# Kernel tuning notes

Measured on AMD Instinct MI355X. Metric: run time of the kernel, lower is better.

Reference implementation:

```python
import math
import jax, jax.numpy as jnp
import numpy as np

B, T, C = 2, 2048, 2048
H, G = 16, 4
D = C // H  # head_dim = 128
KV = G * D
SOFT_CAP = 50.0
EPS = 1e-6


def setup_inputs() -> dict:
    key = jax.random.key(0)
    ks = jax.random.split(key, 5)
    s = 1.0 / math.sqrt(C)
    return {
        "x": jax.random.normal(ks[0], (B, T, C), jnp.float32),
        "Wq": jax.random.normal(ks[1], (C, C), jnp.float32) * s,
        "Wk": jax.random.normal(ks[2], (KV, C), jnp.float32) * s,
        "Wv": jax.random.normal(ks[3], (KV, C), jnp.float32) * s,
        "Wo": jax.random.normal(ks[4], (C, C), jnp.float32) * s,
        "bo": jnp.zeros((C,), jnp.float32),
        "q_norm_w": jnp.ones((D,), jnp.float32),
        "k_norm_w": jnp.ones((D,), jnp.float32),
    }


def _rmsnorm(x, w):
    # norm/sqrt(d) formulation, eps added to rms (matches torch module exactly)
    rms = jnp.linalg.norm(x, axis=-1, keepdims=True) / math.sqrt(x.shape[-1])
    return w * (x / (rms + EPS))


def _rotary_tables(seq_len, dim):
    inv_freq = 1.0 / (10000.0 ** (jnp.arange(0, dim, 2, dtype=jnp.float32) / dim))
    t = jnp.arange(seq_len, dtype=jnp.float32)
    freqs = jnp.outer(t, inv_freq)  # [T, D/2]
    return jnp.cos(freqs), jnp.sin(freqs)


def _apply_rope(x, cos, sin):
    # x: [B, T, h, D]; cos/sin: [T, D/2] broadcast as [1, T, 1, D/2]
    d = x.shape[-1] // 2
    x1, x2 = x[..., :d], x[..., d:]
    c = cos[None, :, None, :]
    s = sin[None, :, None, :]
    return jnp.concatenate([x1 * c + x2 * s, -x1 * s + x2 * c], axis=-1)


def reference(x, Wq, Wk, Wv, Wo, bo, q_norm_w, k_norm_w):
    b, t, c = x.shape
    q = (x @ Wq.T).reshape(b, t, H, D)
    k = (x @ Wk.T).reshape(b, t, G, D)
    v = (x @ Wv.T).reshape(b, t, G, D)

    cos, sin = _rotary_tables(t, D)
    q = _apply_rope(_rmsnorm(q, q_norm_w), cos, sin)
    k = _apply_rope(_rmsnorm(k, k_norm_w), cos, sin)

    q = q.transpose(0, 2, 1, 3)              # [B, H, T, D]
    k = jnp.repeat(k.transpose(0, 2, 1, 3), H // G, axis=1)  # [B, H, T, D]
    v = jnp.repeat(v.transpose(0, 2, 1, 3), H // G, axis=1)

    att = jnp.einsum("bhqd,bhkd->bhqk", q, k) / math.sqrt(D)
    causal = jnp.tril(jnp.ones((t, t), bool))
    att = jnp.where(causal[None, None], att, -jnp.inf)
    att = SOFT_CAP * jnp.tanh(att / SOFT_CAP)  # masked entries -> -50
    att = jax.nn.softmax(att, axis=-1)

    y = jnp.einsum("bhqk,bhkd->bhqd", att, v)
    y = y.transpose(0, 2, 1, 3).reshape(b, t, c)
    return y @ Wo.T + bo
```

## Files before the change

kernel.cpp:

```cpp
#include <hip/hip_runtime.h>
#include <math.h>

#define T_SEQ 2048
#define C_DIM 2048
#define NH    16
#define NG    4
#define DH    128
#define BATCH 2

typedef unsigned short u16;
typedef __bf16 bf16_t;
typedef bf16_t bf16x8 __attribute__((ext_vector_type(8)));
typedef float  f32x4  __attribute__((ext_vector_type(4)));

static __device__ __forceinline__ u16 f2bf(float f) {
    return __builtin_bit_cast(u16, (__bf16)f);
}

static __device__ __forceinline__ void gll16(const void* g, void* lds) {
    __builtin_amdgcn_global_load_lds(
        (const __attribute__((address_space(1))) void*)(unsigned long long)(g),
        (__attribute__((address_space(3))) void*)(unsigned int)(unsigned long long)(lds),
        16, 0, 0);
}

__global__ __launch_bounds__(256)
void cast_multi(const float* __restrict__ x,  const float* __restrict__ wq,
                const float* __restrict__ wk, const float* __restrict__ wv,
                u16* __restrict__ xo, u16* __restrict__ wqo,
                u16* __restrict__ wko, u16* __restrict__ wvo) {
    int i = blockIdx.x * 256 + threadIdx.x;
    const float* src; u16* dst; int off;
    if (i < 1048576)      { src = x;  dst = xo;  off = i; }
    else if (i < 1572864) { src = wq; dst = wqo; off = i - 1048576; }
    else if (i < 1703936) { src = wk; dst = wko; off = i - 1572864; }
    else                  { src = wv; dst = wvo; off = i - 1703936; }
    const float4* p = (const float4*)src + (size_t)off * 2;
    float4 a = p[0], b = p[1];
    u16 u[8] = {f2bf(a.x), f2bf(a.y), f2bf(a.z), f2bf(a.w),
                f2bf(b.x), f2bf(b.y), f2bf(b.z), f2bf(b.w)};
    *(uint4*)(dst + (size_t)off * 8) = *(const uint4*)u;
}

__global__ __launch_bounds__(256)
void cast_f32_bf16(const float* __restrict__ in, u16* __restrict__ out, int n8) {
    int i = blockIdx.x * 256 + threadIdx.x;
    if (i >= n8) return;
    const float4* p = (const float4*)in + (size_t)i * 2;
    float4 a = p[0], b = p[1];
    u16 u[8] = {f2bf(a.x), f2bf(a.y), f2bf(a.z), f2bf(a.w),
                f2bf(b.x), f2bf(b.y), f2bf(b.z), f2bf(b.w)};
    *(uint4*)(out + (size_t)i * 8) = *(const uint4*)u;
}

__global__ __launch_bounds__(256)
void rope_tables(float* __restrict__ cosT, float* __restrict__ sinT) {
    int i = blockIdx.x * 256 + threadIdx.x;
    int tp = i >> 6, ln = i & 63;
    float invfreq = __builtin_amdgcn_exp2f(-(float)ln * (13.287712379549449f / 64.0f));
    float s, c;
    sincosf((float)tp * invfreq, &s, &c);
    cosT[i] = c;
    sinT[i] = s;
}

static __device__ __forceinline__ void gemm_body(
        u16* As, u16* Bs,
        const u16* __restrict__ A, const u16* __restrict__ B,
        const float* __restrict__ bias, float* __restrict__ C,
        int N, int K, int m0, int n0) {
    const int t    = threadIdx.x;
    const int lane = t & 63, w = t >> 6;
    const int l15  = lane & 15, quad = lane >> 4;
    const int wr   = w >> 1, wc = w & 1;

    f32x4 acc[4][4];
#pragma unroll
    for (int mt = 0; mt < 4; ++mt)
#pragma unroll
        for (int nt = 0; nt < 4; ++nt) acc[mt][nt] = (f32x4){0.f, 0.f, 0.f, 0.f};

    const int off0 = w*2048 + lane*16;
    const int r0 = off0 >> 6,          c0 = (off0 & 63) >> 1;
    const int r1 = (off0+1024) >> 6,   c1 = ((off0+1024) & 63) >> 1;
    const u16* Ag0 = A + (size_t)(m0 + r0) * K + c0;
    const u16* Ag1 = A + (size_t)(m0 + r1) * K + c1;
    const u16* Bg0 = B + (size_t)(n0 + r0) * K + c0;
    const u16* Bg1 = B + (size_t)(n0 + r1) * K + c1;
    char* AsB = (char*)As; char* BsB = (char*)Bs;
    const int ldsOff0 = w*2048, ldsOff1 = w*2048 + 1024;

    for (int k0 = 0; k0 < K; k0 += 32) {
        gll16(Ag0 + k0, AsB + ldsOff0);
        gll16(Ag1 + k0, AsB + ldsOff1);
        gll16(Bg0 + k0, BsB + ldsOff0);
        gll16(Bg1 + k0, BsB + ldsOff1);
        __syncthreads();
        bf16x8 af[4], bf[4];
#pragma unroll
        for (int mt = 0; mt < 4; ++mt)
            af[mt] = __builtin_bit_cast(bf16x8,
                *(const uint4*)&As[(wr*64 + mt*16 + l15)*32 + quad*8]);
#pragma unroll
        for (int nt = 0; nt < 4; ++nt)
            bf[nt] = __builtin_bit_cast(bf16x8,
                *(const uint4*)&Bs[(wc*64 + nt*16 + l15)*32 + quad*8]);
#pragma unroll
        for (int mt = 0; mt < 4; ++mt)
#pragma unroll
            for (int nt = 0; nt < 4; ++nt)
                acc[mt][nt] = __builtin_amdgcn_mfma_f32_16x16x32_bf16(
                                  af[mt], bf[nt], acc[mt][nt], 0, 0, 0);
        __syncthreads();
    }

#pragma unroll
    for (int mt = 0; mt < 4; ++mt)
#pragma unroll
        for (int nt = 0; nt < 4; ++nt) {
            const int col = n0 + wc*64 + nt*16 + l15;
            const float bv = bias ? bias[col] : 0.f;
#pragma unroll
            for (int r = 0; r < 4; ++r) {
                const int row = m0 + wr*64 + mt*16 + quad*4 + r;
                C[(size_t)row * N + col] = acc[mt][nt][r] + bv;
            }
        }
}

__global__ __launch_bounds__(256)
void gemm_nt_bf16(const u16* __restrict__ A, const u16* __restrict__ B,
                  const float* __restrict__ bias, float* __restrict__ C,
                  int N, int K) {
    __shared__ __align__(16) u16 As[128*32];
    __shared__ __align__(16) u16 Bs[128*32];
    gemm_body(As, Bs, A, B, bias, C, N, K, blockIdx.y*128, blockIdx.x*128);
}

__global__ __launch_bounds__(256)
void gemm_qkv(const u16* __restrict__ A,  const u16* __restrict__ Bq,
              const u16* __restrict__ Bk, const u16* __restrict__ Bv,
              float* __restrict__ Cq, float* __restrict__ Ck, float* __restrict__ Cv) {
    __shared__ __align__(16) u16 As[128*32];
    __shared__ __align__(16) u16 Bs[128*32];
    const int bx = blockIdx.x;
    const u16* B; float* C; int N, n0;
    if (bx < 16)      { B = Bq; C = Cq; N = 2048; n0 = bx * 128; }
    else if (bx < 20) { B = Bk; C = Ck; N = 512;  n0 = (bx-16) * 128; }
    else              { B = Bv; C = Cv; N = 512;  n0 = (bx-20) * 128; }
    gemm_body(As, Bs, A, B, nullptr, C, N, 2048, blockIdx.y*128, n0);
}

__global__ __launch_bounds__(256)
void rmsnorm_rope_qk(const float* __restrict__ qf, const float* __restrict__ kf,
                     const float* __restrict__ qw, const float* __restrict__ kw,
                     const float* __restrict__ cosT, const float* __restrict__ sinT,
                     u16* __restrict__ qo, u16* __restrict__ ko) {
    const int blk  = blockIdx.x;
    const int sub  = threadIdx.x >> 6;
    const int lane = threadIdx.x & 63;
    const float* in; const float* w; u16* out; int row, nheads; float scale;
    if (blk < 16384) {
        in = qf; w = qw; out = qo; nheads = NH; scale = 0.08838834764831845f;
        row = blk * 4 + sub;
    } else {
        in = kf; w = kw; out = ko; nheads = NG; scale = 1.0f;
        row = (blk - 16384) * 4 + sub;
    }
    const float* p = in + (size_t)row * 128;
    float x1 = p[lane], x2 = p[lane + 64];
    float ss = x1*x1 + x2*x2;
#pragma unroll
    for (int off = 32; off >= 1; off >>= 1) ss += __shfl_xor(ss, off, 64);
    float inv = 1.0f / (sqrtf(ss * (1.0f/128.0f)) + 1e-6f);
    float x1n = w[lane]      * x1 * inv;
    float x2n = w[lane + 64] * x2 * inv;
    int tpos = (row / nheads) & (T_SEQ - 1);
    float c = cosT[tpos*64 + lane];
    float s = sinT[tpos*64 + lane];
    out[(size_t)row*128 + lane]      = f2bf((x1n * c + x2n * s) * scale);
    out[(size_t)row*128 + lane + 64] = f2bf((x2n * c - x1n * s) * scale);
}

__global__ __launch_bounds__(256)
void v_cast_transpose(const float* __restrict__ v, u16* __restrict__ vt) {
    __shared__ u16 Lt[128 * 66];
    const int t  = threadIdx.x;
    const int t0 = blockIdx.x * 64;
    const int bg = blockIdx.y;
    const int b  = bg / NG, g = bg % NG;
#pragma unroll
    for (int rep = 0; rep < 8; ++rep) {
        int idx = rep * 256 + t;
        int i   = idx >> 5;
        int c   = idx & 31;
        float4 f = *(const float4*)(v + ((size_t)(b*T_SEQ + t0 + i)*NG + g)*DH + c*4);
        Lt[(c*4+0)*66 + i] = f2bf(f.x);
        Lt[(c*4+1)*66 + i] = f2bf(f.y);
        Lt[(c*4+2)*66 + i] = f2bf(f.z);
        Lt[(c*4+3)*66 + i] = f2bf(f.w);
    }
    __syncthreads();
#pragma unroll
    for (int rep = 0; rep < 4; ++rep) {
        int idx = rep * 256 + t;
        int d = idx >> 3, c = idx & 7;
        const u16* src = &Lt[d*66 + c*8];
        uint4 val;
        val.x = *(const unsigned int*)(src + 0);
        val.y = *(const unsigned int*)(src + 2);
        val.z = *(const unsigned int*)(src + 4);
        val.w = *(const unsigned int*)(src + 6);
        *(uint4*)(vt + ((size_t)(bg*DH + d))*T_SEQ + t0 + c*8) = val;
    }
}

__global__ __launch_bounds__(256, 2)
void flash_attn_mfma(const u16* __restrict__ qh, const u16* __restrict__ kh,
                     const u16* __restrict__ vt, u16* __restrict__ y) {
    __shared__ __align__(16) u16 Ks[2][64*128];
    __shared__ __align__(16) u16 Vs[2][128*64];

    const int t    = threadIdx.x;
    const int lane = t & 63, w = t >> 6;
    const int l15  = lane & 15, quad = lane >> 4;
    const int bg   = blockIdx.y;
    const int b    = bg >> 2, g = bg & 3;
    const int chunk = b ? (int)blockIdx.x : (63 - (int)blockIdx.x);
    const int q0   = chunk * 32;
    const int h    = g * (NH / NG) + w;

    const float C0 =  1.4426950408889634f;
    const float C1 = -0.48089834696298777f;
    const float C2 =  0.19235933878519512f;
    const float C3 = -0.07785972536301652f;

    bf16x8 aq[2][4];
#pragma unroll
    for (int m = 0; m < 2; ++m) {
        const u16* qp = qh + ((size_t)(b*T_SEQ + q0 + m*16 + l15) * NH + h) * DH;
#pragma unroll
        for (int kc = 0; kc < 4; ++kc)
            aq[m][kc] = __builtin_bit_cast(bf16x8, *(const uint4*)(qp + kc*32 + quad*8));
    }

    f32x4 accO[2][8];
#pragma unroll
    for (int m = 0; m < 2; ++m)
#pragma unroll
        for (int nd = 0; nd < 8; ++nd) accO[m][nd] = (f32x4){0.f, 0.f, 0.f, 0.f};
    float ls[2] = {0.f, 0.f};

    const u16* kgb = kh + ((size_t)b*T_SEQ*NG + g)*DH;
    const u16* vgb = vt + ((size_t)(b*NG + g)*DH)*T_SEQ;

    const int krb = t >> 4, kcl = t & 15;
    const int vdb = t >> 3, vcl = t & 7;

    const int ktiles = q0/64 + 1;

#pragma unroll
    for (int j = 0; j < 4; ++j) {
        const int kr = j*16 + krb;
        const int rp = kr & 31;
        const int kphys = (kr & 32) + ((rp >> 2) & 3)*8 + (rp >> 4)*4 + (rp & 3);
        gll16(kgb + (size_t)kphys*(NG*DH) + ((kcl ^ (kr & 7)) << 3),
              (char*)Ks[0] + j*4096 + w*1024);
        const int vd = j*32 + vdb;
        gll16(vgb + (size_t)vd*T_SEQ + ((vcl ^ (vd & 7)) << 3),
              (char*)Vs[0] + j*4096 + w*1024);
    }

    for (int kt = 0; kt < ktiles; ++kt) {
        asm volatile("s_waitcnt vmcnt(0)" ::: "memory");
        __syncthreads();

        if (kt + 1 < ktiles) {
            const int k0n = (kt + 1) * 64, bn = (kt + 1) & 1;
#pragma unroll
            for (int j = 0; j < 4; ++j) {
                const int kr = j*16 + krb;
                const int rp = kr & 31;
                const int kphys = (kr & 32) + ((rp >> 2) & 3)*8 + (rp >> 4)*4 + (rp & 3);
                gll16(kgb + (size_t)(k0n + kphys)*(NG*DH) + ((kcl ^ (kr & 7)) << 3),
                      (char*)Ks[bn] + j*4096 + w*1024);
                const int vd = j*32 + vdb;
                gll16(vgb + (size_t)vd*T_SEQ + k0n + ((vcl ^ (vd & 7)) << 3),
                      (char*)Vs[bn] + j*4096 + w*1024);
            }
        }

        const u16* Kb = Ks[kt & 1];
        const u16* Vb = Vs[kt & 1];
        const int k0 = kt * 64;
        const bool diag = (kt == ktiles - 1);

        bf16x8 pa[2][2];
#pragma unroll
        for (int b32 = 0; b32 < 2; ++b32) {
            alignas(16) u16 pk0[8];
            alignas(16) u16 pk1[8];
#pragma unroll
            for (int sub = 0; sub < 2; ++sub) {
                const int kc16 = b32*2 + sub;
                const int krow = kc16*16 + l15;
                const int kswz = (krow & 7) << 3;
                f32x4 st0 = (f32x4){0.f,0.f,0.f,0.f};
                f32x4 st1 = (f32x4){0.f,0.f,0.f,0.f};
#pragma unroll
                for (int kc = 0; kc < 4; ++kc) {
                    bf16x8 ak = __builtin_bit_cast(bf16x8,
                        *(const uint4*)&Kb[krow*128 + ((kc*32 + quad*8) ^ kswz)]);
                    st0 = __builtin_amdgcn_mfma_f32_16x16x32_bf16(ak, aq[0][kc], st0, 0, 0, 0);
                    st1 = __builtin_amdgcn_mfma_f32_16x16x32_bf16(ak, aq[1][kc], st1, 0, 0, 0);
                }
#pragma unroll
                for (int m = 0; m < 2; ++m) {
                    const f32x4 st = m ? st1 : st0;
#pragma unroll
                    for (int r = 0; r < 4; ++r) {
                        float sv = st[r];
                        float z = sv * 0.02f;
                        float u = z * z;
                        float poly = fmaf(u, fmaf(u, fmaf(u, C3, C2), C1), C0);
                        float pv = __builtin_amdgcn_exp2f(sv * poly);
                        if (diag) {
                            const int keyg = k0 + b32*32 + quad*8 + sub*4 + r;
                            const int qg   = q0 + m*16 + l15;
                            pv = (keyg > qg) ? 0.f : pv;
                        }
                        ls[m] += pv;
                        if (m) pk1[sub*4 + r] = f2bf(pv);
                        else   pk0[sub*4 + r] = f2bf(pv);
                    }
                }
            }
            pa[0][b32] = __builtin_bit_cast(bf16x8, *(const uint4*)pk0);
            pa[1][b32] = __builtin_bit_cast(bf16x8, *(const uint4*)pk1);
        }

#pragma unroll
        for (int nd = 0; nd < 8; ++nd) {
            const int vrow = nd*16 + l15;
            const int vswz = (vrow & 7) << 3;
#pragma unroll
            for (int b32 = 0; b32 < 2; ++b32) {
                bf16x8 bv = __builtin_bit_cast(bf16x8,
                    *(const uint4*)&Vb[vrow*64 + ((b32*32 + quad*8) ^ vswz)]);
                accO[0][nd] = __builtin_amdgcn_mfma_f32_16x16x32_bf16(pa[0][b32], bv, accO[0][nd], 0, 0, 0);
                accO[1][nd] = __builtin_amdgcn_mfma_f32_16x16x32_bf16(pa[1][b32], bv, accO[1][nd], 0, 0, 0);
            }
        }
    }

#pragma unroll
    for (int m = 0; m < 2; ++m) {
        float v = ls[m];
        v += __shfl_xor(v, 16, 64);
        v += __shfl_xor(v, 32, 64);
        ls[m] = v;
    }

#pragma unroll
    for (int m = 0; m < 2; ++m)
#pragma unroll
        for (int r = 0; r < 4; ++r) {
            const float invl = 1.f / __shfl(ls[m], quad*4 + r, 64);
            u16* yp = y + (size_t)(b*T_SEQ + q0 + m*16 + quad*4 + r) * C_DIM + h*DH;
#pragma unroll
            for (int nd = 0; nd < 8; ++nd)
                yp[nd*16 + l15] = f2bf(accO[m][nd][r] * invl);
        }
}

extern "C" void kernel_launch(void* const* d_in, const int* in_sizes, int n_in,
                              void* d_out, int out_size, void* d_ws, size_t ws_size,
                              hipStream_t stream) {
    const float* x  = (const float*)d_in[0];
    const float* Wq = (const float*)d_in[1];
    const float* Wk = (const float*)d_in[2];
    const float* Wv = (const float*)d_in[3];
    const float* Wo = (const float*)d_in[4];
    const float* bo = (const float*)d_in[5];
    const float* qw = (const float*)d_in[6];
    const float* kw = (const float*)d_in[7];
    float* out = (float*)d_out;

    const size_t qE = (size_t)BATCH * T_SEQ * NH * DH;
    const size_t kE = (size_t)BATCH * T_SEQ * NG * DH;
    const size_t wqE = (size_t)C_DIM * C_DIM;
    const size_t wkE = (size_t)(NG*DH) * C_DIM;

    float* qf  = (float*)d_ws;
    float* kf  = qf + qE;
    float* vf  = kf + kE;
    u16*   qh  = (u16*)(vf + kE);
    u16*   khb = qh + qE;
    u16*   vtb = khb + kE;
    u16*   xh  = vtb + kE;
    u16*   wqh = xh + qE;
    u16*   wkh = wqh + wqE;
    u16*   wvh = wkh + wkE;
    float* cosT = (float*)(wvh + wkE);
    float* sinT = cosT + 131072;
    u16*   woh = (u16*)kf;
    u16*   yh  = (u16*)qf;

    const int M = BATCH * T_SEQ;
    dim3 blk(256);

    rope_tables<<<dim3(512), blk, 0, stream>>>(cosT, sinT);

    cast_multi<<<dim3(7168), blk, 0, stream>>>(x, Wq, Wk, Wv, xh, wqh, wkh, wvh);

    gemm_qkv<<<dim3(24, M/128), blk, 0, stream>>>(xh, wqh, wkh, wvh, qf, kf, vf);

    rmsnorm_rope_qk<<<dim3(M*NH/4 + M*NG/4), blk, 0, stream>>>(qf, kf, qw, kw, cosT, sinT, qh, khb);
    v_cast_transpose<<<dim3(T_SEQ/64, BATCH*NG), blk, 0, stream>>>(vf, vtb);

    cast_f32_bf16<<<dim3(wqE/8/256), blk, 0, stream>>>(Wo, woh, wqE/8);

    flash_attn_mfma<<<dim3(T_SEQ/32, BATCH*NG), blk, 0, stream>>>(qh, khb, vtb, yh);

    gemm_nt_bf16<<<dim3(C_DIM/128, M/128), blk, 0, stream>>>(yh, woh, bo, out, C_DIM, C_DIM);
}
```

Baseline: 320.8 us.

## Fuse RMSNorm and RoPE into QKV GEMM epilogue, emit bf16 V

The QKV GEMM epilogue now applies per-head RMSNorm, RoPE and scaling directly to the accumulators and writes bf16 Q/K. It does this by staging each 16-row slice in LDS so each wave can read the partner half and the cross-wave sum of squares. V is written as bf16 instead of fp32, and the transpose kernel reads bf16. This removes the standalone rmsnorm_rope_qk kernel and the fp32 round trip for the QKV intermediates. The cost is a longer epilogue with extra syncs and LDS traffic, plus uncoalesced 2-byte stores.

```diff
diff --git a/kernel.cpp b/kernel.cpp
--- a/kernel.cpp
+++ b/kernel.cpp
@@ -64,17 +64,15 @@
     sinT[i] = s;
 }
 
-static __device__ __forceinline__ void gemm_body(
+static __device__ __forceinline__ void gemm_core(
         u16* As, u16* Bs,
         const u16* __restrict__ A, const u16* __restrict__ B,
-        const float* __restrict__ bias, float* __restrict__ C,
-        int N, int K, int m0, int n0) {
+        int K, int m0, int n0, f32x4 (&acc)[4][4]) {
     const int t    = threadIdx.x;
     const int lane = t & 63, w = t >> 6;
     const int l15  = lane & 15, quad = lane >> 4;
     const int wr   = w >> 1, wc = w & 1;
 
-    f32x4 acc[4][4];
 #pragma unroll
     for (int mt = 0; mt < 4; ++mt)
 #pragma unroll
@@ -113,19 +111,6 @@
                                   af[mt], bf[nt], acc[mt][nt], 0, 0, 0);
         __syncthreads();
     }
-
-#pragma unroll
-    for (int mt = 0; mt < 4; ++mt)
-#pragma unroll
-        for (int nt = 0; nt < 4; ++nt) {
-            const int col = n0 + wc*64 + nt*16 + l15;
-            const float bv = bias ? bias[col] : 0.f;
-#pragma unroll
-            for (int r = 0; r < 4; ++r) {
-                const int row = m0 + wr*64 + mt*16 + quad*4 + r;
-                C[(size_t)row * N + col] = acc[mt][nt][r] + bv;
-            }
-        }
 }
 
 __global__ __launch_bounds__(256)
@@ -134,71 +119,138 @@
                   int N, int K) {
     __shared__ __align__(16) u16 As[128*32];
     __shared__ __align__(16) u16 Bs[128*32];
-    gemm_body(As, Bs, A, B, bias, C, N, K, blockIdx.y*128, blockIdx.x*128);
+    const int m0 = blockIdx.y*128, n0 = blockIdx.x*128;
+    f32x4 acc[4][4];
+    gemm_core(As, Bs, A, B, K, m0, n0, acc);
+
+    const int t    = threadIdx.x;
+    const int lane = t & 63, w = t >> 6;
+    const int l15  = lane & 15, quad = lane >> 4;
+    const int wr   = w >> 1, wc = w & 1;
+#pragma unroll
+    for (int mt = 0; mt < 4; ++mt)
+#pragma unroll
+        for (int nt = 0; nt < 4; ++nt) {
+            const int col = n0 + wc*64 + nt*16 + l15;
+            const float bv = bias ? bias[col] : 0.f;
+#pragma unroll
+            for (int r = 0; r < 4; ++r) {
+                const int row = m0 + wr*64 + mt*16 + quad*4 + r;
+                C[(size_t)row * N + col] = acc[mt][nt][r] + bv;
+            }
+        }
 }
 
 __global__ __launch_bounds__(256)
 void gemm_qkv(const u16* __restrict__ A,  const u16* __restrict__ Bq,
               const u16* __restrict__ Bk, const u16* __restrict__ Bv,
-              float* __restrict__ Cq, float* __restrict__ Ck, float* __restrict__ Cv) {
-    __shared__ __align__(16) u16 As[128*32];
-    __shared__ __align__(16) u16 Bs[128*32];
+              const float* __restrict__ qw, const float* __restrict__ kw,
+              const float* __restrict__ cosT, const float* __restrict__ sinT,
+              u16* __restrict__ qh, u16* __restrict__ kh, u16* __restrict__ vfh) {
+    __shared__ __align__(16) u16 smem[8448];
+    __shared__ float ssqA[64];
     const int bx = blockIdx.x;
-    const u16* B; float* C; int N, n0;
-    if (bx < 16)      { B = Bq; C = Cq; N = 2048; n0 = bx * 128; }
-    else if (bx < 20) { B = Bk; C = Ck; N = 512;  n0 = (bx-16) * 128; }
-    else              { B = Bv; C = Cv; N = 512;  n0 = (bx-20) * 128; }
-    gemm_body(As, Bs, A, B, nullptr, C, N, 2048, blockIdx.y*128, n0);
-}
-
-__global__ __launch_bounds__(256)
-void rmsnorm_rope_qk(const float* __restrict__ qf, const float* __restrict__ kf,
-                     const float* __restrict__ qw, const float* __restrict__ kw,
-                     const float* __restrict__ cosT, const float* __restrict__ sinT,
-                     u16* __restrict__ qo, u16* __restrict__ ko) {
-    const int blk  = blockIdx.x;
-    const int sub  = threadIdx.x >> 6;
-    const int lane = threadIdx.x & 63;
-    const float* in; const float* w; u16* out; int row, nheads; float scale;
-    if (blk < 16384) {
-        in = qf; w = qw; out = qo; nheads = NH; scale = 0.08838834764831845f;
-        row = blk * 4 + sub;
-    } else {
-        in = kf; w = kw; out = ko; nheads = NG; scale = 1.0f;
-        row = (blk - 16384) * 4 + sub;
-    }
-    const float* p = in + (size_t)row * 128;
-    float x1 = p[lane], x2 = p[lane + 64];
-    float ss = x1*x1 + x2*x2;
-#pragma unroll
-    for (int off = 32; off >= 1; off >>= 1) ss += __shfl_xor(ss, off, 64);
-    float inv = 1.0f / (sqrtf(ss * (1.0f/128.0f)) + 1e-6f);
-    float x1n = w[lane]      * x1 * inv;
-    float x2n = w[lane + 64] * x2 * inv;
-    int tpos = (row / nheads) & (T_SEQ - 1);
-    float c = cosT[tpos*64 + lane];
-    float s = sinT[tpos*64 + lane];
-    out[(size_t)row*128 + lane]      = f2bf((x1n * c + x2n * s) * scale);
-    out[(size_t)row*128 + lane + 64] = f2bf((x2n * c - x1n * s) * scale);
-}
-
-__global__ __launch_bounds__(256)
-void v_cast_transpose(const float* __restrict__ v, u16* __restrict__ vt) {
+    const u16* B; int N, n0, mode;
+    if (bx < 16)      { B = Bq; N = 2048; n0 = bx * 128;      mode = 0; }
+    else if (bx < 20) { B = Bk; N = 512;  n0 = (bx-16) * 128; mode = 1; }
+    else              { B = Bv; N = 512;  n0 = (bx-20) * 128; mode = 2; }
+    const int m0 = blockIdx.y * 128;
+
+    f32x4 acc[4][4];
+    gemm_core(smem, smem + 4096, A, B, 2048, m0, n0, acc);
+
+    const int t    = threadIdx.x;
+    const int lane = t & 63, w = t >> 6;
+    const int l15  = lane & 15, quad = lane >> 4;
+    const int wr   = w >> 1, wc = w & 1;
+
+    if (mode == 2) {
+#pragma unroll
+        for (int mt = 0; mt < 4; ++mt)
+#pragma unroll
+            for (int nt = 0; nt < 4; ++nt) {
+                const int col = n0 + wc*64 + nt*16 + l15;
+#pragma unroll
+                for (int r = 0; r < 4; ++r) {
+                    const int row = m0 + wr*64 + mt*16 + quad*4 + r;
+                    vfh[(size_t)row * 512 + col] = f2bf(acc[mt][nt][r]);
+                }
+            }
+        return;
+    }
+
+    float* Lch = (float*)smem;
+    const float* wn = mode ? kw : qw;
+    u16* outp = mode ? kh : qh;
+    const int nh = mode ? NG : NH;
+    const float scale = mode ? 1.0f : 0.08838834764831845f;
+    const int hh = n0 >> 7;
+
+    for (int mt = 0; mt < 4; ++mt) {
+        float p[4];
+#pragma unroll
+        for (int r = 0; r < 4; ++r) {
+            float s = 0.f;
+#pragma unroll
+            for (int nt = 0; nt < 4; ++nt) {
+                float v = acc[mt][nt][r];
+                Lch[(wr*16 + quad*4 + r)*132 + wc*64 + nt*16 + l15] = v;
+                s = fmaf(v, v, s);
+            }
+            s += __shfl_xor(s, 1, 64);
+            s += __shfl_xor(s, 2, 64);
+            s += __shfl_xor(s, 4, 64);
+            s += __shfl_xor(s, 8, 64);
+            p[r] = s;
+        }
+        if (l15 == 0) {
+#pragma unroll
+            for (int r = 0; r < 4; ++r)
+                ssqA[wr*32 + wc*16 + quad*4 + r] = p[r];
+        }
+        __syncthreads();
+#pragma unroll
+        for (int r = 0; r < 4; ++r) {
+            const int row16 = quad*4 + r;
+            const int rg = m0 + wr*64 + mt*16 + row16;
+            const int tpos = rg & (T_SEQ - 1);
+            const float tot = ssqA[wr*32 + row16] + ssqA[wr*32 + 16 + row16];
+            const float inv = scale / (sqrtf(tot * (1.0f/128.0f)) + 1e-6f);
+            u16* op = outp + ((size_t)rg * nh + hh) * DH;
+#pragma unroll
+            for (int nt = 0; nt < 4; ++nt) {
+                const int dl = nt*16 + l15;
+                const float xo = acc[mt][nt][r];
+                const float xp = Lch[(wr*16 + row16)*132 + (wc^1)*64 + dl];
+                const float xon = wn[wc*64 + dl]     * xo * inv;
+                const float xpn = wn[(wc^1)*64 + dl] * xp * inv;
+                const float c = cosT[tpos*64 + dl];
+                const float s = sinT[tpos*64 + dl];
+                const float val = wc ? (xon*c - xpn*s) : (xon*c + xpn*s);
+                op[wc*64 + dl] = f2bf(val);
+            }
+        }
+        __syncthreads();
+    }
+}
+
+__global__ __launch_bounds__(256)
+void v_cast_transpose(const u16* __restrict__ v, u16* __restrict__ vt) {
     __shared__ u16 Lt[128 * 66];
     const int t  = threadIdx.x;
     const int t0 = blockIdx.x * 64;
     const int bg = blockIdx.y;
     const int b  = bg / NG, g = bg % NG;
 #pragma unroll
-    for (int rep = 0; rep < 8; ++rep) {
+    for (int rep = 0; rep < 4; ++rep) {
         int idx = rep * 256 + t;
-        int i   = idx >> 5;
-        int c   = idx & 31;
-        float4 f = *(const float4*)(v + ((size_t)(b*T_SEQ + t0 + i)*NG + g)*DH + c*4);
-        Lt[(c*4+0)*66 + i] = f2bf(f.x);
-        Lt[(c*4+1)*66 + i] = f2bf(f.y);
-        Lt[(c*4+2)*66 + i] = f2bf(f.z);
-        Lt[(c*4+3)*66 + i] = f2bf(f.w);
+        int i   = idx >> 4;
+        int c   = idx & 15;
+        uint4 vv = *(const uint4*)(v + ((size_t)(b*T_SEQ + t0 + i)*NG + g)*DH + c*8);
+        const u16* pv = (const u16*)&vv;
+#pragma unroll
+        for (int jj = 0; jj < 8; ++jj)
+            Lt[(c*8 + jj)*66 + i] = pv[jj];
     }
     __syncthreads();
 #pragma unroll
@@ -391,20 +443,18 @@
     const size_t wqE = (size_t)C_DIM * C_DIM;
     const size_t wkE = (size_t)(NG*DH) * C_DIM;
 
-    float* qf  = (float*)d_ws;
-    float* kf  = qf + qE;
-    float* vf  = kf + kE;
-    u16*   qh  = (u16*)(vf + kE);
+    u16*   qh  = (u16*)d_ws;
     u16*   khb = qh + qE;
-    u16*   vtb = khb + kE;
+    u16*   vfh = khb + kE;
+    u16*   vtb = vfh + kE;
     u16*   xh  = vtb + kE;
     u16*   wqh = xh + qE;
     u16*   wkh = wqh + wqE;
     u16*   wvh = wkh + wkE;
-    float* cosT = (float*)(wvh + wkE);
+    u16*   woh = wvh + wkE;
+    u16*   yh  = woh + wqE;
+    float* cosT = (float*)(yh + qE);
     float* sinT = cosT + 131072;
-    u16*   woh = (u16*)kf;
-    u16*   yh  = (u16*)qf;
 
     const int M = BATCH * T_SEQ;
     dim3 blk(256);
@@ -412,14 +462,14 @@
     rope_tables<<<dim3(512), blk, 0, stream>>>(cosT, sinT);
 
     cast_multi<<<dim3(7168), blk, 0, stream>>>(x, Wq, Wk, Wv, xh, wqh, wkh, wvh);
-
-    gemm_qkv<<<dim3(24, M/128), blk, 0, stream>>>(xh, wqh, wkh, wvh, qf, kf, vf);
-
-    rmsnorm_rope_qk<<<dim3(M*NH/4 + M*NG/4), blk, 0, stream>>>(qf, kf, qw, kw, cosT, sinT, qh, khb);
-    v_cast_transpose<<<dim3(T_SEQ/64, BATCH*NG), blk, 0, stream>>>(vf, vtb);
-
     cast_f32_bf16<<<dim3(wqE/8/256), blk, 0, stream>>>(Wo, woh, wqE/8);
 
+    gemm_qkv<<<dim3(24, M/128), blk, 0, stream>>>(xh, wqh, wkh, wvh,
+                                                  qw, kw, cosT, sinT,
+                                                  qh, khb, vfh);
+
+    v_cast_transpose<<<dim3(T_SEQ/64, BATCH*NG), blk, 0, stream>>>(vfh, vtb);
+
     flash_attn_mfma<<<dim3(T_SEQ/32, BATCH*NG), blk, 0, stream>>>(qh, khb, vtb, yh);
 
     gemm_nt_bf16<<<dim3(C_DIM/128, M/128), blk, 0, stream>>>(yh, woh, bo, out, C_DIM, C_DIM);
```

Result: slower. 385.7 us (+20.3%).
